# Kernel optimization log

Hardware: AMD Instinct MI355X
Metric: run time of the kernel (lower is better)

Reference implementation:

```python
import jax, jax.numpy as jnp
import numpy as np

DIM = 2048
N_HEADS = 16
HEAD_DIM = DIM // N_HEADS
HIDDEN = 8192
BSZ = 2
SEQ = 2048
EPS = 1e-6


def setup_inputs() -> dict:
    key = jax.random.key(0)
    ks = jax.random.split(key, 8)
    x = jax.random.normal(ks[0], (BSZ, SEQ, DIM), dtype=jnp.float32)
    # causal additive mask, broadcastable to [B, H, S, S]
    mask = jnp.where(jnp.tril(jnp.ones((SEQ, SEQ), dtype=bool)), 0.0, -1e9)
    mask = mask[None, None, :, :].astype(jnp.float32)
    s = 0.02
    # torch.nn.Linear weights have shape [out_features, in_features]
    wq = jax.random.normal(ks[1], (DIM, DIM), dtype=jnp.float32) * s
    wk = jax.random.normal(ks[2], (DIM, DIM), dtype=jnp.float32) * s
    wv = jax.random.normal(ks[3], (DIM, DIM), dtype=jnp.float32) * s
    wo = jax.random.normal(ks[4], (DIM, DIM), dtype=jnp.float32) * s
    w1 = jax.random.normal(ks[5], (HIDDEN, DIM), dtype=jnp.float32) * s
    w2 = jax.random.normal(ks[6], (DIM, HIDDEN), dtype=jnp.float32) * s
    attn_norm_w = jnp.ones((DIM,), dtype=jnp.float32)
    ffn_norm_w = jnp.ones((DIM,), dtype=jnp.float32)
    return {"x": x, "mask": mask, "wq": wq, "wk": wk, "wv": wv, "wo": wo,
            "w1": w1, "w2": w2, "attn_norm_w": attn_norm_w, "ffn_norm_w": ffn_norm_w}


def rmsnorm(x, w):
    return x * jax.lax.rsqrt(jnp.mean(x * x, axis=-1, keepdims=True) + EPS) * w


def attention(x, mask, wq, wk, wv, wo):
    b, s, _ = x.shape
    q = (x @ wq.T).reshape(b, s, N_HEADS, HEAD_DIM)
    k = (x @ wk.T).reshape(b, s, N_HEADS, HEAD_DIM)
    v = (x @ wv.T).reshape(b, s, N_HEADS, HEAD_DIM)
    scores = jnp.einsum('bqhd,bkhd->bhqk', q, k) / jnp.sqrt(jnp.float32(HEAD_DIM))
    scores = scores + mask
    probs = jax.nn.softmax(scores, axis=-1)
    out = jnp.einsum('bhqk,bkhd->bqhd', probs, v).reshape(b, s, DIM)
    return out @ wo.T


def reference(x, mask, wq, wk, wv, wo, w1, w2, attn_norm_w, ffn_norm_w):
    h = x + attention(rmsnorm(x, attn_norm_w), mask, wq, wk, wv, wo)
    ffn_in = rmsnorm(h, ffn_norm_w)
    ffn = jax.nn.relu(ffn_in @ w1.T) @ w2.T
    return h + ffn
```

## Files before the change

### kernel.cpp

```cpp
#include <hip/hip_runtime.h>
#include <cstdint>
#include <cstddef>

#define DIM 2048
#define NHEADS 16
#define HD 128
#define HIDDEN 8192
#define BSZ 2
#define SEQ 2048
#define MTOT (BSZ*SEQ)

typedef __bf16 bf16_t;
typedef __bf16 bf16x8 __attribute__((ext_vector_type(8)));
typedef __bf16 bf16x4 __attribute__((ext_vector_type(4)));
typedef float  f32x4  __attribute__((ext_vector_type(4)));

__device__ __forceinline__ void gload16(const void* g, void* lds) {
  __builtin_amdgcn_global_load_lds(
      (const __attribute__((address_space(1))) uint32_t*)g,
      (__attribute__((address_space(3))) uint32_t*)lds, 16, 0, 0);
}

#define BAR() do { __builtin_amdgcn_sched_barrier(0); \
  asm volatile("s_barrier" ::: "memory"); \
  __builtin_amdgcn_sched_barrier(0); } while (0)
#define VMW(N) asm volatile("s_waitcnt vmcnt(" #N ")" ::: "memory")

__global__ void cvt_all_k(const float* __restrict__ wq, const float* __restrict__ wk,
                          const float* __restrict__ wv, const float* __restrict__ wo,
                          const float* __restrict__ w1, const float* __restrict__ w2,
                          bf16_t* __restrict__ dst) {
  const int S1 = (DIM*DIM) >> 2;
  const int S2 = (DIM*HIDDEN) >> 2;
  const int total = 4*S1 + 2*S2;
  int i = blockIdx.x * blockDim.x + threadIdx.x;
  const int stride = gridDim.x * blockDim.x;
  for (; i < total; i += stride) {
    const float* src; int off;
    if (i < 4*S1) {
      const int r = i >> 20; off = i & (S1 - 1);
      src = (r == 0) ? wq : (r == 1) ? wk : (r == 2) ? wv : wo;
    } else {
      const int j = i - 4*S1;
      if (j < S2) { src = w1; off = j; } else { src = w2; off = j - S2; }
    }
    float4 v = ((const float4*)src)[off];
    bf16x4 o = {(__bf16)v.x, (__bf16)v.y, (__bf16)v.z, (__bf16)v.w};
    ((bf16x4*)dst)[i] = o;
  }
}

__global__ __launch_bounds__(256)
void rmsnorm_k(const float* __restrict__ x, const float* __restrict__ wt,
               bf16_t* __restrict__ out) {
  const int row = blockIdx.x;
  const float* xr = x + (size_t)row * DIM;
  const int tid = threadIdx.x;
  float4 a = ((const float4*)xr)[tid];
  float4 b = ((const float4*)xr)[tid + 256];
  float ss = a.x*a.x + a.y*a.y + a.z*a.z + a.w*a.w
           + b.x*b.x + b.y*b.y + b.z*b.z + b.w*b.w;
  #pragma unroll
  for (int d = 32; d >= 1; d >>= 1) ss += __shfl_xor(ss, d, 64);
  __shared__ float red[4];
  if ((tid & 63) == 0) red[tid >> 6] = ss;
  __syncthreads();
  float tot = red[0] + red[1] + red[2] + red[3];
  float rs = rsqrtf(tot * (1.0f / DIM) + 1e-6f);
  float4 wa = ((const float4*)wt)[tid];
  float4 wb = ((const float4*)wt)[tid + 256];
  bf16x4 oa = {(__bf16)(a.x*rs*wa.x), (__bf16)(a.y*rs*wa.y),
               (__bf16)(a.z*rs*wa.z), (__bf16)(a.w*rs*wa.w)};
  bf16x4 ob = {(__bf16)(b.x*rs*wb.x), (__bf16)(b.y*rs*wb.y),
               (__bf16)(b.z*rs*wb.z), (__bf16)(b.w*rs*wb.w)};
  *(bf16x4*)(out + (size_t)row*DIM + tid*4)        = oa;
  *(bf16x4*)(out + (size_t)row*DIM + 1024 + tid*4) = ob;
}

template<int MH, int NH>
__device__ __forceinline__ void mm16(f32x4 (&acc)[8][4],
                                     const bf16x8 (&aF)[4][2],
                                     const bf16x8 (&bF)[2][2]) {
  __builtin_amdgcn_s_setprio(1);
  #pragma unroll
  for (int mt = 0; mt < 4; ++mt)
    #pragma unroll
    for (int nt = 0; nt < 2; ++nt)
      #pragma unroll
      for (int kk = 0; kk < 2; ++kk)
        acc[MH*4+mt][NH*2+nt] = __builtin_amdgcn_mfma_f32_16x16x32_bf16(
            aF[mt][kk], bF[nt][kk], acc[MH*4+mt][NH*2+nt], 0, 0, 0);
  __builtin_amdgcn_s_setprio(0);
}

__device__ __forceinline__ void rdA4(bf16x8 (&aF)[4][2], const bf16_t* rbase,
                                     int wr, int l16, int g) {
  #pragma unroll
  for (int mt = 0; mt < 4; ++mt)
    #pragma unroll
    for (int kk = 0; kk < 2; ++kk)
      aF[mt][kk] = *(const bf16x8*)((const char*)rbase +
          (wr*64 + mt*16 + l16)*128 + ((((kk<<2) ^ g) ^ (l16 & 7)) << 4));
}
__device__ __forceinline__ void rdB2(bf16x8 (&bF)[2][2], const bf16_t* rbase,
                                     int wc, int l16, int g) {
  #pragma unroll
  for (int nt = 0; nt < 2; ++nt)
    #pragma unroll
    for (int kk = 0; kk < 2; ++kk)
      bF[nt][kk] = *(const bf16x8*)((const char*)rbase +
          (wc*32 + nt*16 + l16)*128 + ((((kk<<2) ^ g) ^ (l16 & 7)) << 4));
}

template<typename OUT_T, bool RELU, bool HAS_RES>
__global__ __launch_bounds__(512, 2)
void gemm8p(const bf16_t* __restrict__ A, const bf16_t* __restrict__ B,
            OUT_T* __restrict__ C, const float* __restrict__ res,
            int M, int N, int K) {
  __shared__ bf16_t sA[2][2][128*64];
  __shared__ bf16_t sB[2][2][128*64];
  const int tid  = threadIdx.x;
  const int lane = tid & 63;
  const int wid  = tid >> 6;
  const int l16  = lane & 15;
  const int g    = lane >> 4;
  const int wr   = wid >> 2;
  const int wc   = wid & 3;

  const int nwg = gridDim.x, bid = blockIdx.x;
  const int qq = nwg >> 3, rr = nwg & 7;
  const int xcd = bid & 7, loc = bid >> 3;
  const int wg = (xcd < rr ? xcd*(qq+1) : rr*(qq+1) + (xcd-rr)*qq) + loc;
  const int nbn = N >> 8;
  const int bm = (wg / nbn) << 8;
  const int bn = (wg % nbn) << 8;

  const int lr  = tid >> 3;
  const int cq8 = (((tid & 7) ^ (lr & 7)) << 3);

  const size_t aR = (size_t)(bm + lr) * K + cq8;
  const size_t bR = (size_t)(bn + ((lr >> 5) << 6) + (lr & 31)) * K + cq8;
  const size_t rowK128 = (size_t)128 * K, rowK64 = (size_t)64 * K, rowK32 = (size_t)32 * K;

  auto stA = [&](int buf, int mh, int kt) {
    const size_t ko = aR + (size_t)kt * 64 + (size_t)mh * rowK64;
    gload16(A + ko,            &sA[buf][mh][wid*512]);
    gload16(A + ko + rowK128,  &sA[buf][mh][4096 + wid*512]);
  };
  auto stB = [&](int buf, int nh, int kt) {
    const size_t ko = bR + (size_t)kt * 64 + (size_t)nh * rowK32;
    gload16(B + ko,              &sB[buf][nh][wid*512]);
    gload16(B + ko + 2*rowK64,   &sB[buf][nh][4096 + wid*512]);
  };

  f32x4 acc[8][4] = {};
  bf16x8 aF[4][2], bLo[2][2], bHi[2][2];

  stA(0, 0, 0); stB(0, 0, 0); stB(0, 1, 0); stA(0, 1, 0);
  stA(1, 0, 1); stB(1, 0, 1); stB(1, 1, 1);
  VMW(6);
  BAR();

  const int ni = K >> 7;
  for (int j = 0; j < ni; ++j) {
    const int t1 = 2*j + 1, t2 = 2*j + 2, t3 = 2*j + 3;
    const bool more = (j + 1 < ni);
    rdA4(aF, &sA[0][0][0], wr, l16, g);
    rdB2(bLo, &sB[0][0][0], wc, l16, g);
    stA(1, 1, t1);
    BAR();
    mm16<0,0>(acc, aF, bLo);
    BAR();
    rdB2(bHi, &sB[0][1][0], wc, l16, g);
    if (more) stA(0, 0, t2);
    BAR();
    mm16<0,1>(acc, aF, bHi);
    BAR();
    rdA4(aF, &sA[0][1][0], wr, l16, g);
    if (more) stB(0, 0, t2);
    BAR();
    mm16<1,1>(acc, aF, bHi);
    BAR();
    if (more) { stB(0, 1, t2); VMW(6); } else { VMW(0); }
    BAR();
    mm16<1,0>(acc, aF, bLo);
    BAR();
    rdA4(aF, &sA[1][0][0], wr, l16, g);
    rdB2(bLo, &sB[1][0][0], wc, l16, g);
    if (more) stA(0, 1, t2);
    BAR();
    mm16<0,0>(acc, aF, bLo);
    BAR();
    rdB2(bHi, &sB[1][1][0], wc, l16, g);
    if (more) stA(1, 0, t3);
    BAR();
    mm16<0,1>(acc, aF, bHi);
    BAR();
    rdA4(aF, &sA[1][1][0], wr, l16, g);
    if (more) stB(1, 0, t3);
    BAR();
    mm16<1,1>(acc, aF, bHi);
    BAR();
    if (more) { stB(1, 1, t3); VMW(6); }
    BAR();
    mm16<1,0>(acc, aF, bLo);
    BAR();
  }

  #pragma unroll
  for (int am = 0; am < 8; ++am) {
    #pragma unroll
    for (int r = 0; r < 4; ++r) {
      const int row = bm + wr*128 + am*16 + g*4 + r;
      #pragma unroll
      for (int an = 0; an < 4; ++an) {
        const int col = bn + wc*64 + an*16 + l16;
        float v = acc[am][an][r];
        if (HAS_RES) v += res[(size_t)row * N + col];
        if (RELU)    v = fmaxf(v, 0.0f);
        C[(size_t)row * N + col] = (OUT_T)v;
      }
    }
  }
}

template<int MH, int NH>
__device__ __forceinline__ void mm8(f32x4 (&acc)[4][4],
                                    const bf16x8 (&aF)[2][2],
                                    const bf16x8 (&bF)[2][2]) {
  __builtin_amdgcn_s_setprio(1);
  #pragma unroll
  for (int mt = 0; mt < 2; ++mt)
    #pragma unroll
    for (int nt = 0; nt < 2; ++nt)
      #pragma unroll
      for (int kk = 0; kk < 2; ++kk)
        acc[MH*2+mt][NH*2+nt] = __builtin_amdgcn_mfma_f32_16x16x32_bf16(
            aF[mt][kk], bF[nt][kk], acc[MH*2+mt][NH*2+nt], 0, 0, 0);
  __builtin_amdgcn_s_setprio(0);
}

__device__ __forceinline__ void rd2(bf16x8 (&f)[2][2], const bf16_t* rbase,
                                    int wrow, int l16, int g) {
  #pragma unroll
  for (int t = 0; t < 2; ++t)
    #pragma unroll
    for (int kk = 0; kk < 2; ++kk)
      f[t][kk] = *(const bf16x8*)((const char*)rbase +
          (wrow + t*16 + l16)*128 + ((((kk<<2) ^ g) ^ (l16 & 7)) << 4));
}

template<typename OUT_T, bool RELU, bool HAS_RES, int OMODE>
__global__ __launch_bounds__(512, 2)
void gemm8p_n128(const bf16_t* __restrict__ A, const bf16_t* __restrict__ B,
                 OUT_T* __restrict__ C, const float* __restrict__ res,
                 int M, int N, int K) {
  __shared__ bf16_t sA[2][2][128*64];
  __shared__ bf16_t sB[2][2][64*64];
  const int tid  = threadIdx.x;
  const int lane = tid & 63;
  const int wid  = tid >> 6;
  const int l16  = lane & 15;
  const int g    = lane >> 4;
  const int wr   = wid >> 1;
  const int wc   = wid & 1;

  const int nwg = gridDim.x, bid = blockIdx.x;
  const int qq = nwg >> 3, rr = nwg & 7;
  const int xcd = bid & 7, loc = bid >> 3;
  const int wg = (xcd < rr ? xcd*(qq+1) : rr*(qq+1) + (xcd-rr)*qq) + loc;
  const int nbn = N >> 7;
  const int bm = (wg / nbn) << 8;
  const int bn = (wg % nbn) << 7;

  const int lr  = tid >> 3;
  const int cq8 = (((tid & 7) ^ (lr & 7)) << 3);
  const size_t aR = (size_t)(bm + ((lr >> 5) << 6) + (lr & 31)) * K + cq8;
  const size_t bR = (size_t)(bn + ((lr >> 5) << 6) + (lr & 31)) * K + cq8;
  const size_t rowK128 = (size_t)128 * K, rowK32 = (size_t)32 * K;

  auto stA = [&](int buf, int mh, int kt) {
    const size_t ko = aR + (size_t)kt * 64 + (size_t)mh * rowK32;
    gload16(A + ko,            &sA[buf][mh][wid*512]);
    gload16(A + ko + rowK128,  &sA[buf][mh][4096 + wid*512]);
  };
  auto stB = [&](int buf, int nh, int kt) {
    gload16(B + bR + (size_t)kt * 64 + (size_t)nh * rowK32, &sB[buf][nh][wid*512]);
  };

  f32x4 acc[4][4] = {};
  bf16x8 aF[2][2], bLo[2][2], bHi[2][2];

  stA(0, 0, 0); stB(0, 0, 0); stB(0, 1, 0); stA(0, 1, 0);
  stA(1, 0, 1); stB(1, 0, 1); stB(1, 1, 1);
  VMW(4);
  BAR();

  const int ar = wr*32;
  const int br = wc*32;
  const int ni = K >> 7;
  for (int j = 0; j < ni; ++j) {
    const int t1 = 2*j + 1, t2 = 2*j + 2, t3 = 2*j + 3;
    const bool more = (j + 1 < ni);
    rd2(aF,  &sA[0][0][0], ar, l16, g);
    rd2(bLo, &sB[0][0][0], br, l16, g);
    stA(1, 1, t1);
    BAR();
    mm8<0,0>(acc, aF, bLo);
    BAR();
    rd2(bHi, &sB[0][1][0], br, l16, g);
    if (more) stA(0, 0, t2);
    BAR();
    mm8<0,1>(acc, aF, bHi);
    BAR();
    rd2(aF, &sA[0][1][0], ar, l16, g);
    if (more) stB(0, 0, t2);
    BAR();
    mm8<1,1>(acc, aF, bHi);
    BAR();
    if (more) { stB(0, 1, t2); VMW(4); } else { VMW(0); }
    BAR();
    mm8<1,0>(acc, aF, bLo);
    BAR();
    rd2(aF,  &sA[1][0][0], ar, l16, g);
    rd2(bLo, &sB[1][0][0], br, l16, g);
    if (more) stA(0, 1, t2);
    BAR();
    mm8<0,0>(acc, aF, bLo);
    BAR();
    rd2(bHi, &sB[1][1][0], br, l16, g);
    if (more) stA(1, 0, t3);
    BAR();
    mm8<0,1>(acc, aF, bHi);
    BAR();
    rd2(aF, &sA[1][1][0], ar, l16, g);
    if (more) stB(1, 0, t3);
    BAR();
    mm8<1,1>(acc, aF, bHi);
    BAR();
    if (more) { stB(1, 1, t3); VMW(4); }
    BAR();
    mm8<1,0>(acc, aF, bLo);
    BAR();
  }

  if (OMODE == 2) {
    const int t = bn >> 11;
    const int clb = bn & 2047;
    if (t < 2) {
      bf16_t* base = (bf16_t*)C + (size_t)t * MTOT * DIM;
      #pragma unroll
      for (int am = 0; am < 4; ++am) {
        #pragma unroll
        for (int r = 0; r < 4; ++r) {
          const int row = bm + wr*64 + am*16 + g*4 + r;
          #pragma unroll
          for (int an = 0; an < 4; ++an) {
            const int cl = clb + wc*64 + an*16 + l16;
            base[(size_t)row * DIM + cl] = (bf16_t)acc[am][an][r];
          }
        }
      }
    } else {
      bf16_t* vbase = (bf16_t*)C + (size_t)2 * MTOT * DIM;
      #pragma unroll
      for (int am = 0; am < 4; ++am) {
        const int row = bm + wr*64 + am*16 + g*4;
        #pragma unroll
        for (int an = 0; an < 4; ++an) {
          const int cl = clb + wc*64 + an*16 + l16;
          f32x4 a4 = acc[am][an];
          bf16x4 v4 = {(__bf16)a4[0], (__bf16)a4[1], (__bf16)a4[2], (__bf16)a4[3]};
          *(bf16x4*)(vbase +
              (((size_t)(row >> 11) * NHEADS + (cl >> 7)) * HD + (cl & 127)) * SEQ
              + (row & 2047)) = v4;
        }
      }
    }
  } else {
    #pragma unroll
    for (int am = 0; am < 4; ++am) {
      #pragma unroll
      for (int r = 0; r < 4; ++r) {
        const int row = bm + wr*64 + am*16 + g*4 + r;
        #pragma unroll
        for (int an = 0; an < 4; ++an) {
          const int col = bn + wc*64 + an*16 + l16;
          float v = acc[am][an][r];
          if (HAS_RES) v += res[(size_t)row * N + col];
          if (RELU)    v = fmaxf(v, 0.0f);
          C[(size_t)row * N + col] = (OUT_T)v;
        }
      }
    }
  }
}

__global__ __launch_bounds__(256, 2)
void attn_k(const bf16_t* __restrict__ Q, const bf16_t* __restrict__ Kk,
            const bf16_t* __restrict__ VT, bf16_t* __restrict__ O) {
  __shared__ bf16_t sK[2][64 * 128];
  __shared__ bf16_t sVT[2][128 * 64];
  __shared__ bf16_t sP[4][32 * 64];
  const int tid = threadIdx.x, lane = tid & 63, w = tid >> 6;
  const int l16 = lane & 15, g = lane >> 4;
  const int b = blockIdx.z, h = blockIdx.y;
  const int qt = b ? (SEQ/128 - 1 - blockIdx.x) : blockIdx.x;
  const int ch = h * HD;
  const size_t gb = (size_t)b * SEQ * DIM;
  const int qbase = qt*128 + w*32;
  const bf16_t* VTh = VT + ((size_t)b * NHEADS + h) * ((size_t)HD * SEQ);

  bf16x8 qf[2][4];
  #pragma unroll
  for (int mt = 0; mt < 2; ++mt)
    #pragma unroll
    for (int kb = 0; kb < 4; ++kb)
      qf[mt][kb] = *(const bf16x8*)(Q + gb + (size_t)(qbase + mt*16 + l16)*DIM + ch + kb*32 + g*8);

  const float qs = 0.08838834764831845f * 1.44269504088896f;
  #pragma unroll
  for (int mt = 0; mt < 2; ++mt)
    #pragma unroll
    for (int kb = 0; kb < 4; ++kb)
      #pragma unroll
      for (int e = 0; e < 8; ++e)
        qf[mt][kb][e] = (__bf16)((float)qf[mt][kb][e] * qs);

  f32x4 o[2][8] = {};
  float l_r[2][4];
  #pragma unroll
  for (int mt = 0; mt < 2; ++mt)
    #pragma unroll
    for (int r = 0; r < 4; ++r) l_r[mt][r] = 0.0f;

  const int nsteps = (qt*128 + 128) >> 6;

  auto stageK = [&](int buf, int kv0) {
    #pragma unroll
    for (int i = 0; i < 4; ++i) {
      const int c = i*256 + tid;
      const int kv = c >> 4, pos = c & 15;
      const int qsrc = pos ^ (kv & 7);
      gload16(Kk + gb + (size_t)(kv0 + kv)*DIM + ch + (qsrc << 3),
              (char*)sK[buf] + (size_t)(i*256 + w*64)*16);
    }
  };
  auto stageVT = [&](int buf, int kv0) {
    #pragma unroll
    for (int i = 0; i < 4; ++i) {
      const int c = i*256 + tid;
      const int d = c >> 3, p = c & 7;
      const int q = p ^ (d & 7);
      gload16(VTh + (size_t)d * SEQ + kv0 + (q << 3),
              (char*)sVT[buf] + (size_t)(i*256 + w*64)*16);
    }
  };

  stageK(0, 0);  stageVT(0, 0);
  if (nsteps > 1) { stageK(1, 64); stageVT(1, 64); }
  __syncthreads();

  int cur = 0;
  for (int t = 0; t < nsteps; ++t) {
    const int kv0 = t << 6;
    const bool active = (kv0 < qbase + 32);
    if (active) {
      f32x4 s[2][4] = {};
      const char* kb_ = (const char*)sK[cur];
      __builtin_amdgcn_s_setprio(1);
      #pragma unroll
      for (int nt = 0; nt < 4; ++nt) {
        const int row = nt*16 + l16;
        #pragma unroll
        for (int kbi = 0; kbi < 4; ++kbi) {
          const int pos = (kbi*4 + g) ^ (l16 & 7);
          bf16x8 kf = *(const bf16x8*)(kb_ + row*256 + (pos << 4));
          #pragma unroll
          for (int mt = 0; mt < 2; ++mt)
            s[mt][nt] = __builtin_amdgcn_mfma_f32_16x16x32_bf16(qf[mt][kbi], kf, s[mt][nt], 0, 0, 0);
        }
      }
      __builtin_amdgcn_s_setprio(0);

      const bool needmask = (kv0 + 63 > qbase);
      char* pb = (char*)sP[w];
      #pragma unroll
      for (int mt = 0; mt < 2; ++mt) {
        #pragma unroll
        for (int r = 0; r < 4; ++r) {
          const int qpos = qbase + mt*16 + g*4 + r;
          float p[4], rsum = 0.0f;
          #pragma unroll
          for (int nt = 0; nt < 4; ++nt) {
            float sv = s[mt][nt][r];
            if (needmask && (kv0 + nt*16 + l16 > qpos)) sv = -1e9f;
            p[nt] = exp2f(sv);
            rsum += p[nt];
          }
          #pragma unroll
          for (int d = 8; d >= 1; d >>= 1) rsum += __shfl_xor(rsum, d, 16);
          l_r[mt][r] += rsum;
          const int prow = mt*16 + g*4 + r;
          #pragma unroll
          for (int nt = 0; nt < 4; ++nt)
            *(bf16_t*)(pb + ((prow*128 + nt*32 + l16*2) ^ (g << 5))) = (bf16_t)p[nt];
        }
      }

      bf16x8 pa[2][2];
      #pragma unroll
      for (int mt = 0; mt < 2; ++mt) {
        const int row2 = mt*16 + l16;
        #pragma unroll
        for (int ks = 0; ks < 2; ++ks)
          pa[mt][ks] = *(const bf16x8*)((const char*)sP[w] +
                    ((row2*128 + ks*64 + g*16) ^ (((l16 >> 2) & 3) << 5)));
      }

      const char* vb_ = (const char*)sVT[cur];
      __builtin_amdgcn_s_setprio(1);
      #pragma unroll
      for (int dt = 0; dt < 8; ++dt) {
        const int d = dt*16 + l16;
        #pragma unroll
        for (int ks = 0; ks < 2; ++ks) {
          const int pos = (ks*4 + g) ^ (d & 7);
          bf16x8 vf = *(const bf16x8*)(vb_ + d*128 + (pos << 4));
          #pragma unroll
          for (int mt = 0; mt < 2; ++mt)
            o[mt][dt] = __builtin_amdgcn_mfma_f32_16x16x32_bf16(pa[mt][ks], vf, o[mt][dt], 0, 0, 0);
        }
      }
      __builtin_amdgcn_s_setprio(0);
    }
    __syncthreads();
    if (t + 2 < nsteps) {
      stageK(cur, (t + 2) << 6);
      stageVT(cur, (t + 2) << 6);
    }
    cur ^= 1;
  }

  #pragma unroll
  for (int mt = 0; mt < 2; ++mt) {
    #pragma unroll
    for (int r = 0; r < 4; ++r) {
      const float inv = 1.0f / l_r[mt][r];
      const int row = qbase + mt*16 + g*4 + r;
      #pragma unroll
      for (int dt = 0; dt < 8; ++dt)
        O[gb + (size_t)row*DIM + ch + dt*16 + l16] = (bf16_t)(o[mt][dt][r] * inv);
    }
  }
}

extern "C" void kernel_launch(void* const* d_in, const int* in_sizes, int n_in,
                              void* d_out, int out_size, void* d_ws, size_t ws_size,
                              hipStream_t stream) {
  const float* x   = (const float*)d_in[0];
  const float* wq  = (const float*)d_in[2];
  const float* wk  = (const float*)d_in[3];
  const float* wv  = (const float*)d_in[4];
  const float* wo  = (const float*)d_in[5];
  const float* w1  = (const float*)d_in[6];
  const float* w2  = (const float*)d_in[7];
  const float* anw = (const float*)d_in[8];
  const float* fnw = (const float*)d_in[9];
  float* out = (float*)d_out;

  char* p = (char*)d_ws;
  bf16_t* wqb = (bf16_t*)p; p += (size_t)DIM*DIM*2*4;
  bf16_t* w1b = (bf16_t*)p; p += (size_t)DIM*HIDDEN*2;
  bf16_t* w2b = (bf16_t*)p; p += (size_t)DIM*HIDDEN*2;
  bf16_t* xn  = (bf16_t*)p; p += (size_t)MTOT*DIM*2;
  float*  hb  = (float*)p;  p += (size_t)MTOT*DIM*4;
  bf16_t* big = (bf16_t*)p; p += (size_t)MTOT*HIDDEN*2;

  bf16_t* wob = wqb + 3*(size_t)DIM*DIM;
  bf16_t* qb = big;
  bf16_t* kb = big + (size_t)MTOT*DIM;
  bf16_t* vT = big + 2*(size_t)MTOT*DIM;
  bf16_t* ab = big + 3*(size_t)MTOT*DIM;
  bf16_t* f1 = big;

  cvt_all_k<<<4096, 256, 0, stream>>>(wq, wk, wv, wo, w1, w2, wqb);

  rmsnorm_k<<<MTOT, 256, 0, stream>>>(x, anw, xn);

  gemm8p_n128<bf16_t, false, false, 2><<<768, 512, 0, stream>>>(
      xn, wqb, qb, nullptr, MTOT, 3*DIM, DIM);

  attn_k<<<dim3(SEQ/128, NHEADS, BSZ), 256, 0, stream>>>(qb, kb, vT, ab);

  gemm8p_n128<float, false, true, 0><<<256, 512, 0, stream>>>(
      ab, wob, hb, x, MTOT, DIM, DIM);

  rmsnorm_k<<<MTOT, 256, 0, stream>>>(hb, fnw, xn);

  gemm8p<bf16_t, true, false><<<512, 512, 0, stream>>>(
      xn, w1b, f1, nullptr, MTOT, HIDDEN, DIM);

  gemm8p_n128<float, false, true, 0><<<256, 512, 0, stream>>>(
      f1, w2b, out, hb, MTOT, DIM, HIDDEN);
}
```

Baseline: 609.0 us.

## Fuse first rmsnorm into weight conversion and store residual h in bf16

Merges the initial rmsnorm launch into the weight-conversion kernel by giving the extra blocks the row-norm work, which removes one kernel launch. The intermediate residual h is now stored in bf16 instead of fp32. The second rmsnorm reads bf16 with 8-wide vector loads, and the final GEMM adds a bf16 residual through a new OMODE 3 path. This cuts memory traffic for h but adds rounding error on the residual stream that reaches the output.

After: 611.1 us. About the same (+0.4%).

```diff
diff --git a/kernel.cpp b/kernel.cpp
--- a/kernel.cpp
+++ b/kernel.cpp
@@ -26,15 +26,43 @@
   __builtin_amdgcn_sched_barrier(0); } while (0)
 #define VMW(N) asm volatile("s_waitcnt vmcnt(" #N ")" ::: "memory")
 
-__global__ void cvt_all_k(const float* __restrict__ wq, const float* __restrict__ wk,
-                          const float* __restrict__ wv, const float* __restrict__ wo,
-                          const float* __restrict__ w1, const float* __restrict__ w2,
-                          bf16_t* __restrict__ dst) {
+__global__ __launch_bounds__(256)
+void cvtrms_k(const float* __restrict__ x, const float* __restrict__ wt,
+              bf16_t* __restrict__ xn,
+              const float* __restrict__ wq, const float* __restrict__ wk,
+              const float* __restrict__ wv, const float* __restrict__ wo,
+              const float* __restrict__ w1, const float* __restrict__ w2,
+              bf16_t* __restrict__ wdst) {
+  const int tid = threadIdx.x;
+  if (blockIdx.x < MTOT) {
+    const int row = blockIdx.x;
+    const float* xr = x + (size_t)row * DIM;
+    float4 a = ((const float4*)xr)[tid];
+    float4 b = ((const float4*)xr)[tid + 256];
+    float ss = a.x*a.x + a.y*a.y + a.z*a.z + a.w*a.w
+             + b.x*b.x + b.y*b.y + b.z*b.z + b.w*b.w;
+    #pragma unroll
+    for (int d = 32; d >= 1; d >>= 1) ss += __shfl_xor(ss, d, 64);
+    __shared__ float red[4];
+    if ((tid & 63) == 0) red[tid >> 6] = ss;
+    __syncthreads();
+    float tot = red[0] + red[1] + red[2] + red[3];
+    float rs = rsqrtf(tot * (1.0f / DIM) + 1e-6f);
+    float4 wa = ((const float4*)wt)[tid];
+    float4 wb = ((const float4*)wt)[tid + 256];
+    bf16x4 oa = {(__bf16)(a.x*rs*wa.x), (__bf16)(a.y*rs*wa.y),
+                 (__bf16)(a.z*rs*wa.z), (__bf16)(a.w*rs*wa.w)};
+    bf16x4 ob = {(__bf16)(b.x*rs*wb.x), (__bf16)(b.y*rs*wb.y),
+                 (__bf16)(b.z*rs*wb.z), (__bf16)(b.w*rs*wb.w)};
+    *(bf16x4*)(xn + (size_t)row*DIM + tid*4)        = oa;
+    *(bf16x4*)(xn + (size_t)row*DIM + 1024 + tid*4) = ob;
+    return;
+  }
   const int S1 = (DIM*DIM) >> 2;
   const int S2 = (DIM*HIDDEN) >> 2;
   const int total = 4*S1 + 2*S2;
-  int i = blockIdx.x * blockDim.x + threadIdx.x;
-  const int stride = gridDim.x * blockDim.x;
+  int i = (blockIdx.x - MTOT) * blockDim.x + tid;
+  const int stride = (gridDim.x - MTOT) * blockDim.x;
   for (; i < total; i += stride) {
     const float* src; int off;
     if (i < 4*S1) {
@@ -46,20 +74,20 @@
     }
     float4 v = ((const float4*)src)[off];
     bf16x4 o = {(__bf16)v.x, (__bf16)v.y, (__bf16)v.z, (__bf16)v.w};
-    ((bf16x4*)dst)[i] = o;
+    ((bf16x4*)wdst)[i] = o;
   }
 }
 
 __global__ __launch_bounds__(256)
-void rmsnorm_k(const float* __restrict__ x, const float* __restrict__ wt,
-               bf16_t* __restrict__ out) {
+void rmsnorm_bf_k(const bf16_t* __restrict__ h, const float* __restrict__ wt,
+                  bf16_t* __restrict__ out) {
   const int row = blockIdx.x;
-  const float* xr = x + (size_t)row * DIM;
   const int tid = threadIdx.x;
-  float4 a = ((const float4*)xr)[tid];
-  float4 b = ((const float4*)xr)[tid + 256];
-  float ss = a.x*a.x + a.y*a.y + a.z*a.z + a.w*a.w
-           + b.x*b.x + b.y*b.y + b.z*b.z + b.w*b.w;
+  bf16x8 v = *(const bf16x8*)(h + (size_t)row*DIM + tid*8);
+  float f[8];
+  float ss = 0.0f;
+  #pragma unroll
+  for (int e = 0; e < 8; ++e) { f[e] = (float)v[e]; ss += f[e]*f[e]; }
   #pragma unroll
   for (int d = 32; d >= 1; d >>= 1) ss += __shfl_xor(ss, d, 64);
   __shared__ float red[4];
@@ -67,14 +95,14 @@
   __syncthreads();
   float tot = red[0] + red[1] + red[2] + red[3];
   float rs = rsqrtf(tot * (1.0f / DIM) + 1e-6f);
-  float4 wa = ((const float4*)wt)[tid];
-  float4 wb = ((const float4*)wt)[tid + 256];
-  bf16x4 oa = {(__bf16)(a.x*rs*wa.x), (__bf16)(a.y*rs*wa.y),
-               (__bf16)(a.z*rs*wa.z), (__bf16)(a.w*rs*wa.w)};
-  bf16x4 ob = {(__bf16)(b.x*rs*wb.x), (__bf16)(b.y*rs*wb.y),
-               (__bf16)(b.z*rs*wb.z), (__bf16)(b.w*rs*wb.w)};
-  *(bf16x4*)(out + (size_t)row*DIM + tid*4)        = oa;
-  *(bf16x4*)(out + (size_t)row*DIM + 1024 + tid*4) = ob;
+  float4 wa = ((const float4*)wt)[tid*2];
+  float4 wb = ((const float4*)wt)[tid*2 + 1];
+  bf16x8 o;
+  o[0] = (__bf16)(f[0]*rs*wa.x); o[1] = (__bf16)(f[1]*rs*wa.y);
+  o[2] = (__bf16)(f[2]*rs*wa.z); o[3] = (__bf16)(f[3]*rs*wa.w);
+  o[4] = (__bf16)(f[4]*rs*wb.x); o[5] = (__bf16)(f[5]*rs*wb.y);
+  o[6] = (__bf16)(f[6]*rs*wb.z); o[7] = (__bf16)(f[7]*rs*wb.w);
+  *(bf16x8*)(out + (size_t)row*DIM + tid*8) = o;
 }
 
 template<int MH, int NH>
@@ -253,7 +281,7 @@
 template<typename OUT_T, bool RELU, bool HAS_RES, int OMODE>
 __global__ __launch_bounds__(512, 2)
 void gemm8p_n128(const bf16_t* __restrict__ A, const bf16_t* __restrict__ B,
-                 OUT_T* __restrict__ C, const float* __restrict__ res,
+                 OUT_T* __restrict__ C, const void* __restrict__ resv,
                  int M, int N, int K) {
   __shared__ bf16_t sA[2][2][128*64];
   __shared__ bf16_t sB[2][2][64*64];
@@ -378,6 +406,8 @@
       }
     }
   } else {
+    const float* resf = (const float*)resv;
+    const bf16_t* resb = (const bf16_t*)resv;
     #pragma unroll
     for (int am = 0; am < 4; ++am) {
       #pragma unroll
@@ -387,7 +417,10 @@
         for (int an = 0; an < 4; ++an) {
           const int col = bn + wc*64 + an*16 + l16;
           float v = acc[am][an][r];
-          if (HAS_RES) v += res[(size_t)row * N + col];
+          if (HAS_RES) {
+            if (OMODE == 3) v += (float)resb[(size_t)row * N + col];
+            else            v += resf[(size_t)row * N + col];
+          }
           if (RELU)    v = fmaxf(v, 0.0f);
           C[(size_t)row * N + col] = (OUT_T)v;
         }
@@ -574,7 +607,7 @@
   bf16_t* w1b = (bf16_t*)p; p += (size_t)DIM*HIDDEN*2;
   bf16_t* w2b = (bf16_t*)p; p += (size_t)DIM*HIDDEN*2;
   bf16_t* xn  = (bf16_t*)p; p += (size_t)MTOT*DIM*2;
-  float*  hb  = (float*)p;  p += (size_t)MTOT*DIM*4;
+  bf16_t* hb  = (bf16_t*)p; p += (size_t)MTOT*DIM*2;
   bf16_t* big = (bf16_t*)p; p += (size_t)MTOT*HIDDEN*2;
 
   bf16_t* wob = wqb + 3*(size_t)DIM*DIM;
@@ -584,23 +617,21 @@
   bf16_t* ab = big + 3*(size_t)MTOT*DIM;
   bf16_t* f1 = big;
 
-  cvt_all_k<<<4096, 256, 0, stream>>>(wq, wk, wv, wo, w1, w2, wqb);
-
-  rmsnorm_k<<<MTOT, 256, 0, stream>>>(x, anw, xn);
+  cvtrms_k<<<MTOT + 4096, 256, 0, stream>>>(x, anw, xn, wq, wk, wv, wo, w1, w2, wqb);
 
   gemm8p_n128<bf16_t, false, false, 2><<<768, 512, 0, stream>>>(
       xn, wqb, qb, nullptr, MTOT, 3*DIM, DIM);
 
   attn_k<<<dim3(SEQ/128, NHEADS, BSZ), 256, 0, stream>>>(qb, kb, vT, ab);
 
-  gemm8p_n128<float, false, true, 0><<<256, 512, 0, stream>>>(
+  gemm8p_n128<bf16_t, false, true, 0><<<256, 512, 0, stream>>>(
       ab, wob, hb, x, MTOT, DIM, DIM);
 
-  rmsnorm_k<<<MTOT, 256, 0, stream>>>(hb, fnw, xn);
+  rmsnorm_bf_k<<<MTOT, 256, 0, stream>>>(hb, fnw, xn);
 
   gemm8p<bf16_t, true, false><<<512, 512, 0, stream>>>(
       xn, w1b, f1, nullptr, MTOT, HIDDEN, DIM);
 
-  gemm8p_n128<float, false, true, 0><<<256, 512, 0, stream>>>(
+  gemm8p_n128<float, false, true, 3><<<256, 512, 0, stream>>>(
       f1, w2b, out, hb, MTOT, DIM, HIDDEN);
 }
```
